# Optimization experiments

Hardware: AMD Instinct MI355X
Metric: run time of the kernel (lower is better)

The kernel has to match this reference:

```python
import jax, jax.numpy as jnp
import numpy as np

EMBED_DIM = 384
NUM_HEADS = 8
HEAD_DIM = EMBED_DIM // NUM_HEADS
GRN_EPS = 1e-6
LN_EPS = 1e-5


def grn(x, gamma, beta):
    # x: [B,C,H,W]; L2 norm over spatial dims per channel
    gx = jnp.sqrt(jnp.sum(x * x, axis=(-2, -1), keepdims=True))  # [B,C,1,1]
    nx = gx / (jnp.mean(gx, axis=-3, keepdims=True) + GRN_EPS)
    g = gamma[:, None, None]
    b = beta[:, None, None]
    return (1.0 + g) * (x * nx) + b + x


def layernorm(x, w, b):
    mu = jnp.mean(x, axis=-1, keepdims=True)
    var = jnp.mean(jnp.square(x - mu), axis=-1, keepdims=True)
    return (x - mu) * jax.lax.rsqrt(var + LN_EPS) * w + b


def setup_inputs() -> dict:
    key = jax.random.key(0)
    ks = jax.random.split(key, 16)
    C = EMBED_DIM
    B, Hq, Wq, Hk, Wk = 8, 64, 64, 32, 32
    s = 0.02
    inp = {
        "query_img": jax.random.normal(ks[0], (B, C, Hq, Wq), jnp.float32),
        "key_img": jax.random.normal(ks[1], (B, C, Hk, Wk), jnp.float32),
        "value_img": jax.random.normal(ks[2], (B, C, Hk, Wk), jnp.float32),
        "ada_gamma": jnp.zeros((C,), jnp.float32),
        "ada_beta": jnp.zeros((C,), jnp.float32),
        "Wq": jax.random.normal(ks[3], (C, C), jnp.float32) * s,
        "bq": jnp.zeros((C,), jnp.float32),
        "Wk": jax.random.normal(ks[4], (C, C), jnp.float32) * s,
        "bk": jnp.zeros((C,), jnp.float32),
        "Wv": jax.random.normal(ks[5], (C, C), jnp.float32) * s,
        "bv": jnp.zeros((C,), jnp.float32),
        "Wo": jax.random.normal(ks[6], (C, C), jnp.float32) * s,
        "bo": jnp.zeros((C,), jnp.float32),
        "lnq_w": jnp.ones((C,), jnp.float32),
        "lnq_b": jnp.zeros((C,), jnp.float32),
        "lnk_w": jnp.ones((C,), jnp.float32),
        "lnk_b": jnp.zeros((C,), jnp.float32),
        "attn_scalar": jnp.ones((C,), jnp.float32),
        "ffn_gamma": jnp.zeros((C,), jnp.float32),
        "ffn_beta": jnp.zeros((C,), jnp.float32),
        "W1": jax.random.normal(ks[7], (4 * C, C), jnp.float32) * s,
        "b1": jnp.zeros((4 * C,), jnp.float32),
        "W2": jax.random.normal(ks[8], (C, 4 * C), jnp.float32) * s,
        "b2": jnp.zeros((C,), jnp.float32),
        "ffn_scalar": jnp.ones((C,), jnp.float32),
        "final_scalar": jnp.ones((C,), jnp.float32) * 0.1,
    }
    return inp


def reference(query_img, key_img, value_img, ada_gamma, ada_beta, Wq, bq, Wk, bk,
              Wv, bv, Wo, bo, lnq_w, lnq_b, lnk_w, lnk_b, attn_scalar,
              ffn_gamma, ffn_beta, W1, b1, W2, b2, ffn_scalar, final_scalar):
    B, C, Hq, Wq_ = query_img.shape
    Nq = Hq * Wq_
    Nk = key_img.shape[2] * key_img.shape[3]
    H, D = NUM_HEADS, HEAD_DIM

    working = query_img
    ada = grn(working, ada_gamma, ada_beta)

    q_flat = ada.reshape(B, C, Nq).transpose(0, 2, 1)        # [B,Nq,C]
    k_flat = key_img.reshape(B, C, Nk).transpose(0, 2, 1)    # [B,Nk,C]
    v_flat = value_img.reshape(B, C, Nk).transpose(0, 2, 1)  # [B,Nk,C]

    q = layernorm(q_flat @ Wq.T + bq, lnq_w, lnq_b)
    k = layernorm(k_flat @ Wk.T + bk, lnk_w, lnk_b)
    v = v_flat @ Wv.T + bv

    q = (jax.nn.elu(q) + 1.0).reshape(B, Nq, H, D)
    k = (jax.nn.elu(k) + 1.0).reshape(B, Nk, H, D)
    v = v.reshape(B, Nk, H, D)

    kv_sum = jnp.einsum('bnhd,bnhe->bhde', k, v)   # [B,H,D,D]
    k_sum = jnp.sum(k, axis=1)                      # [B,H,D]
    num = jnp.einsum('bqhd,bhde->bqhe', q, kv_sum)  # [B,Nq,H,D]
    den = jnp.einsum('bqhd,bhd->bqh', q, k_sum)[..., None] + 1e-8
    attn = (num / den).reshape(B, Nq, C)
    attn = attn @ Wo.T + bo
    attn_out = attn.transpose(0, 2, 1).reshape(B, C, Hq, Wq_)

    working = working + attn_out * attn_scalar[None, :, None, None]

    normed = grn(working, ffn_gamma, ffn_beta)
    h = jnp.einsum('bchw,fc->bfhw', normed, W1) + b1[None, :, None, None]
    h = jax.nn.silu(h)
    ffn_out = jnp.einsum('bfhw,cf->bchw', h, W2) + b2[None, :, None, None]

    working = working + ffn_out * ffn_scalar[None, :, None, None]
    return query_img + working * final_scalar[None, :, None, None]
```

## Files before the change

### kernel.cpp

```cpp
#include <hip/hip_runtime.h>
#include <hip/hip_bf16.h>
#include <cmath>

typedef __hip_bfloat16 bf16;
typedef __attribute__((ext_vector_type(8))) short s16x8;
typedef __attribute__((ext_vector_type(4))) float f32x4;

#define B_  8
#define C_  384
#define NQ  4096
#define NK  1024
#define NH  8
#define HD  48
#define F_  1536

__device__ __forceinline__ float bits2f(short s) {
    unsigned int u = ((unsigned int)(unsigned short)s) << 16;
    float f; __builtin_memcpy(&f, &u, 4); return f;
}
__device__ __forceinline__ short f2bits(float f) {
    bf16 h = __float2bfloat16(f);
    short s; __builtin_memcpy(&s, &h, 2); return s;
}

__device__ __forceinline__ void gload16(const bf16* g, bf16* l) {
    __builtin_amdgcn_global_load_lds(
        (const __attribute__((address_space(1))) void*)g,
        (__attribute__((address_space(3))) void*)l, 16, 0, 0);
}

__global__ __launch_bounds__(256)
void grn_gx(const float* __restrict__ x, float* __restrict__ gx, int nsp)
{
    size_t base = (size_t)blockIdx.x * nsp;
    float s = 0.0f;
    for (int i = threadIdx.x * 4; i < nsp; i += 256 * 4) {
        float4 v = *reinterpret_cast<const float4*>(&x[base + i]);
        s += v.x * v.x + v.y * v.y + v.z * v.z + v.w * v.w;
    }
    for (int m = 32; m; m >>= 1) s += __shfl_xor(s, m);
    __shared__ float sh[4];
    if ((threadIdx.x & 63) == 0) sh[threadIdx.x >> 6] = s;
    __syncthreads();
    if (threadIdx.x == 0) gx[blockIdx.x] = sqrtf(sh[0] + sh[1] + sh[2] + sh[3]);
}

__global__ __launch_bounds__(384)
void grn_scale(const float* __restrict__ gx, const float* __restrict__ gamma,
               float* __restrict__ scale)
{
    int b = blockIdx.x;
    int c = threadIdx.x;
    float g = gx[b * C_ + c];
    float s = g;
    for (int m = 32; m; m >>= 1) s += __shfl_xor(s, m);
    __shared__ float sh[6];
    if ((c & 63) == 0) sh[c >> 6] = s;
    __syncthreads();
    if (c == 0) {
        float t = 0.0f;
        for (int i = 0; i < 6; ++i) t += sh[i];
        sh[0] = t / (float)C_;
    }
    __syncthreads();
    float nx = g / (sh[0] + 1e-6f);
    scale[b * C_ + c] = (1.0f + gamma[c]) * nx + 1.0f;
}

__global__ __launch_bounds__(256)
void cvt_bf16(const float* __restrict__ src, bf16* __restrict__ dst, int n)
{
    int i = (blockIdx.x * 256 + threadIdx.x) * 8;
    if (i >= n) return;
    float4 a = *reinterpret_cast<const float4*>(src + i);
    float4 b = *reinterpret_cast<const float4*>(src + i + 4);
    s16x8 o;
    o[0] = f2bits(a.x); o[1] = f2bits(a.y); o[2] = f2bits(a.z); o[3] = f2bits(a.w);
    o[4] = f2bits(b.x); o[5] = f2bits(b.y); o[6] = f2bits(b.z); o[7] = f2bits(b.w);
    *reinterpret_cast<s16x8*>(dst + i) = o;
}

template<bool SCALED>
__global__ __launch_bounds__(256)
void t2b(const float* __restrict__ src, bf16* __restrict__ dst,
         const float* __restrict__ scale, const float* __restrict__ shift, int Msp)
{
    const int b = blockIdx.z, c0 = blockIdx.y * 64, m0 = blockIdx.x * 64;
    __shared__ float T[64][65];
    const int tr = threadIdx.x >> 6, tc = threadIdx.x & 63;
    const float* sp = src + ((size_t)b * C_ + c0) * Msp + m0;
#pragma unroll
    for (int i = 0; i < 16; ++i)
        T[i * 4 + tr][tc] = sp[(size_t)(i * 4 + tr) * Msp + tc];
    __syncthreads();
    const int c = c0 + tc;
    float scl = 1.0f, sh = 0.0f;
    if constexpr (SCALED) { scl = scale[b * C_ + c]; sh = shift[c]; }
    bf16* dp = dst + ((size_t)b * Msp + m0) * C_ + c;
#pragma unroll
    for (int i = 0; i < 16; ++i) {
        int m = i * 4 + tr;
        dp[(size_t)m * C_] = __float2bfloat16(T[tc][m] * scl + sh);
    }
}

template<int EPI>
__global__ __launch_bounds__(256)
void gemm_mfma(const bf16* __restrict__ A, const bf16* __restrict__ W,
               const float* __restrict__ bias, int N, int K, int Mspat,
               bf16* __restrict__ outB, float* __restrict__ outF,
               const float* __restrict__ query,
               const float* __restrict__ sc1, const float* __restrict__ sc2)
{
    __shared__ __align__(16) char smem_raw[33792];
    const int tid  = threadIdx.x;
    const int lane = tid & 63, wave = tid >> 6;
    const int wm = wave >> 1, wn = wave & 1;
    const int lrow = lane & 15, lk8 = lane >> 4;
    const int mrow0 = blockIdx.x * 128;
    const int nt    = blockIdx.y * 128;

    const int r0   = wave * 32;
    const int srow = r0 + (lane >> 2);
    const int sk   = (lane & 3) * 8;
    const bf16* Ag = A + (size_t)(mrow0 + srow) * K + sk;
    const bf16* Wg = W + (size_t)(nt    + srow) * K + sk;
    f32x4 acc[4][4] = {};

    auto stage = [&](int p, int kt) {
        bf16* AsD = (bf16*)(smem_raw + p * 16384) + r0 * 32;
        bf16* BsD = (bf16*)(smem_raw + p * 16384 + 8192) + r0 * 32;
        gload16(Ag + kt,                  AsD);
        gload16(Ag + kt + (size_t)16 * K, AsD + 16 * 32);
        gload16(Wg + kt,                  BsD);
        gload16(Wg + kt + (size_t)16 * K, BsD + 16 * 32);
    };
    auto compute = [&](int p) {
        const bf16* As = (const bf16*)(smem_raw + p * 16384);
        const bf16* Bs = (const bf16*)(smem_raw + p * 16384 + 8192);
        s16x8 af[4], bfr[4];
#pragma unroll
        for (int m = 0; m < 4; ++m)
            af[m] = *reinterpret_cast<const s16x8*>(As + (wm * 64 + m * 16 + lrow) * 32 + lk8 * 8);
#pragma unroll
        for (int n = 0; n < 4; ++n)
            bfr[n] = *reinterpret_cast<const s16x8*>(Bs + (wn * 64 + n * 16 + lrow) * 32 + lk8 * 8);
#pragma unroll
        for (int m = 0; m < 4; ++m)
#pragma unroll
            for (int n = 0; n < 4; ++n)
                acc[m][n] = __builtin_amdgcn_mfma_f32_16x16x32_bf16(af[m], bfr[n], acc[m][n], 0, 0, 0);
    };

    stage(0, 0);
    stage(1, 32);
    int cur = 0;
    for (int kt = 0; kt < K - 32; kt += 32) {
        asm volatile("s_waitcnt vmcnt(4)" ::: "memory");
        __builtin_amdgcn_sched_barrier(0);
        __builtin_amdgcn_s_barrier();
        compute(cur);
        __builtin_amdgcn_s_barrier();
        if (kt + 64 < K) stage(cur, kt + 64);
        cur ^= 1;
    }
    asm volatile("s_waitcnt vmcnt(0)" ::: "memory");
    __builtin_amdgcn_sched_barrier(0);
    __builtin_amdgcn_s_barrier();
    compute(cur);
    __syncthreads();

    if constexpr (EPI <= 1) {
        bf16* Cs = (bf16*)smem_raw;
#pragma unroll
        for (int m = 0; m < 4; ++m)
#pragma unroll
            for (int n = 0; n < 4; ++n) {
                int col = wn * 64 + n * 16 + lrow;
                float bv = bias[nt + col];
#pragma unroll
                for (int j = 0; j < 4; ++j) {
                    int row = wm * 64 + m * 16 + lk8 * 4 + j;
                    float v = acc[m][n][j] + bv;
                    if constexpr (EPI == 1) v = v / (1.0f + __expf(-v));
                    Cs[row * 128 + col] = __float2bfloat16(v);
                }
            }
        __syncthreads();
#pragma unroll
        for (int p = 0; p < 8; ++p) {
            int e = p * 256 + tid;
            int row = e >> 4, ch = (e & 15) * 8;
            *reinterpret_cast<s16x8*>(outB + (size_t)(mrow0 + row) * N + nt + ch) =
                *reinterpret_cast<const s16x8*>(Cs + row * 128 + ch);
        }
    } else {
        float* Cs2 = (float*)smem_raw;
        const int b = mrow0 / Mspat;
        const int mloc0 = mrow0 - b * Mspat;
        for (int half = 0; half < 2; ++half) {
            if (half) __syncthreads();
            if (wn == half) {
#pragma unroll
                for (int m = 0; m < 4; ++m)
#pragma unroll
                    for (int n = 0; n < 4; ++n) {
                        int crow = n * 16 + lrow;
                        float bv = bias[nt + half * 64 + crow];
#pragma unroll
                        for (int j = 0; j < 4; ++j) {
                            int mcol = wm * 64 + m * 16 + lk8 * 4 + j;
                            Cs2[crow * 132 + mcol] = acc[m][n][j] + bv;
                        }
                    }
            }
            __syncthreads();
#pragma unroll
            for (int p = 0; p < 8; ++p) {
                int e = p * 256 + tid;
                int crow = e >> 5, m4 = (e & 31) * 4;
                int c = nt + half * 64 + crow;
                size_t off = ((size_t)b * C_ + c) * Mspat + mloc0 + m4;
                float4 v  = *reinterpret_cast<const float4*>(Cs2 + crow * 132 + m4);
                float4 q4 = *reinterpret_cast<const float4*>(query + off);
                float s1 = sc1[c];
                float4 o;
                if constexpr (EPI == 2) {
                    o.x = q4.x + v.x * s1;
                    o.y = q4.y + v.y * s1;
                    o.z = q4.z + v.z * s1;
                    o.w = q4.w + v.w * s1;
                } else {
                    float4 w4 = *reinterpret_cast<const float4*>(outF + off);
                    float s2 = sc2[c];
                    o.x = q4.x + (w4.x + v.x * s1) * s2;
                    o.y = q4.y + (w4.y + v.y * s1) * s2;
                    o.z = q4.z + (w4.z + v.z * s1) * s2;
                    o.w = q4.w + (w4.w + v.w * s1) * s2;
                }
                *reinterpret_cast<float4*>(outF + off) = o;
            }
        }
    }
}

__global__ __launch_bounds__(256)
void ln_elu_b(bf16* __restrict__ x, const float* __restrict__ w,
              const float* __restrict__ bb)
{
    int lane = threadIdx.x & 63, wid = threadIdx.x >> 6;
    int row = blockIdx.x * 4 + wid;
    bf16* p = x + (size_t)row * C_;
    float v[6];
#pragma unroll
    for (int i = 0; i < 6; ++i) v[i] = __bfloat162float(p[lane + i * 64]);
    float s = 0.0f;
#pragma unroll
    for (int i = 0; i < 6; ++i) s += v[i];
    for (int m = 32; m; m >>= 1) s += __shfl_xor(s, m);
    float mu = s / (float)C_;
    float vs = 0.0f;
#pragma unroll
    for (int i = 0; i < 6; ++i) { float d = v[i] - mu; vs += d * d; }
    for (int m = 32; m; m >>= 1) vs += __shfl_xor(vs, m);
    float inv = rsqrtf(vs / (float)C_ + 1e-5f);
#pragma unroll
    for (int i = 0; i < 6; ++i) {
        int c = lane + i * 64;
        float y = (v[i] - mu) * inv * w[c] + bb[c];
        p[c] = __float2bfloat16((y > 0.0f) ? (y + 1.0f) : __expf(y));
    }
}

__global__ __launch_bounds__(256)
void kv_reduce(const bf16* __restrict__ kn, const bf16* __restrict__ vn,
               float* __restrict__ kv, float* __restrict__ ksum)
{
    const int h = blockIdx.x, b = blockIdx.y;
    __shared__ float Ks[128][48];
    __shared__ float Vs[128][48];
    const int t = threadIdx.x;
    const int d0 = (t >> 4) * 3, e0 = (t & 15) * 3;
    float acc[3][3] = {};
    float ks[3] = {};
    for (int n0 = 0; n0 < NK; n0 += 128) {
        for (int ch = t; ch < 768; ch += 256) {
            int r = ch / 6, cc = (ch % 6) * 8;
            size_t base = ((size_t)(b * NK + n0 + r)) * C_ + h * HD + cc;
            s16x8 k8 = *reinterpret_cast<const s16x8*>(kn + base);
            s16x8 v8 = *reinterpret_cast<const s16x8*>(vn + base);
#pragma unroll
            for (int j = 0; j < 8; ++j) {
                Ks[r][cc + j] = bits2f(k8[j]);
                Vs[r][cc + j] = bits2f(v8[j]);
            }
        }
        __syncthreads();
#pragma unroll 4
        for (int r = 0; r < 128; ++r) {
            float k0 = Ks[r][d0], k1 = Ks[r][d0 + 1], k2 = Ks[r][d0 + 2];
            float v0 = Vs[r][e0], v1 = Vs[r][e0 + 1], v2 = Vs[r][e0 + 2];
            acc[0][0] = fmaf(k0, v0, acc[0][0]);
            acc[0][1] = fmaf(k0, v1, acc[0][1]);
            acc[0][2] = fmaf(k0, v2, acc[0][2]);
            acc[1][0] = fmaf(k1, v0, acc[1][0]);
            acc[1][1] = fmaf(k1, v1, acc[1][1]);
            acc[1][2] = fmaf(k1, v2, acc[1][2]);
            acc[2][0] = fmaf(k2, v0, acc[2][0]);
            acc[2][1] = fmaf(k2, v1, acc[2][1]);
            acc[2][2] = fmaf(k2, v2, acc[2][2]);
            if (e0 == 0) { ks[0] += k0; ks[1] += k1; ks[2] += k2; }
        }
        __syncthreads();
    }
    size_t base = (size_t)(b * NH + h) * HD;
#pragma unroll
    for (int i = 0; i < 3; ++i)
#pragma unroll
        for (int j = 0; j < 3; ++j)
            kv[(base + d0 + i) * HD + e0 + j] = acc[i][j];
    if (e0 == 0) {
#pragma unroll
        for (int i = 0; i < 3; ++i) ksum[base + d0 + i] = ks[i];
    }
}

__global__ __launch_bounds__(64)
void attn_numden(const bf16* __restrict__ q, const float* __restrict__ kv,
                 const float* __restrict__ ksum, bf16* __restrict__ attn)
{
    const int nc = blockIdx.x, h = blockIdx.y, b = blockIdx.z;
    __shared__ float skv[48 * 48];
    __shared__ float kss[48];
    const int t = threadIdx.x;
    const float* kvp = kv + (size_t)(b * NH + h) * HD * HD;
    for (int i = t; i < HD * HD; i += 64) skv[i] = kvp[i];
    if (t < HD) kss[t] = ksum[(size_t)(b * NH + h) * HD + t];
    __syncthreads();

    const int n = nc * 64 + t;
    const bf16* qp = q + ((size_t)b * NQ + n) * C_ + h * HD;
    float qv[48];
#pragma unroll
    for (int i = 0; i < 6; ++i) {
        s16x8 v = *reinterpret_cast<const s16x8*>(qp + i * 8);
#pragma unroll
        for (int j = 0; j < 8; ++j) qv[i * 8 + j] = bits2f(v[j]);
    }
    float num[48] = {};
    float den = 0.0f;
#pragma unroll 4
    for (int d = 0; d < 48; ++d) {
        float qd = qv[d];
        den = fmaf(qd, kss[d], den);
#pragma unroll
        for (int e = 0; e < 48; ++e) num[e] = fmaf(qd, skv[d * 48 + e], num[e]);
    }
    float inv = 1.0f / (den + 1e-8f);
    bf16* ap = attn + ((size_t)b * NQ + n) * C_ + h * HD;
#pragma unroll
    for (int i = 0; i < 6; ++i) {
        s16x8 o;
#pragma unroll
        for (int j = 0; j < 8; ++j) o[j] = f2bits(num[i * 8 + j] * inv);
        *reinterpret_cast<s16x8*>(ap + i * 8) = o;
    }
}

extern "C" void kernel_launch(void* const* d_in, const int* in_sizes, int n_in,
                              void* d_out, int out_size, void* d_ws, size_t ws_size,
                              hipStream_t stream)
{
    const float* query       = (const float*)d_in[0];
    const float* key         = (const float*)d_in[1];
    const float* value       = (const float*)d_in[2];
    const float* ada_gamma   = (const float*)d_in[3];
    const float* ada_beta    = (const float*)d_in[4];
    const float* Wq          = (const float*)d_in[5];
    const float* bq          = (const float*)d_in[6];
    const float* Wk          = (const float*)d_in[7];
    const float* bk          = (const float*)d_in[8];
    const float* Wv          = (const float*)d_in[9];
    const float* bv          = (const float*)d_in[10];
    const float* Wo          = (const float*)d_in[11];
    const float* bo          = (const float*)d_in[12];
    const float* lnq_w       = (const float*)d_in[13];
    const float* lnq_b       = (const float*)d_in[14];
    const float* lnk_w       = (const float*)d_in[15];
    const float* lnk_b       = (const float*)d_in[16];
    const float* attn_scalar = (const float*)d_in[17];
    const float* ffn_gamma   = (const float*)d_in[18];
    const float* ffn_beta    = (const float*)d_in[19];
    const float* W1          = (const float*)d_in[20];
    const float* b1          = (const float*)d_in[21];
    const float* W2          = (const float*)d_in[22];
    const float* b2          = (const float*)d_in[23];
    const float* ffn_scalar  = (const float*)d_in[24];
    const float* final_scalar= (const float*)d_in[25];
    float* out = (float*)d_out;

    float* ws    = (float*)d_ws;
    bf16* qbuf   = (bf16*)(ws);
    bf16* attnb  = (bf16*)(ws + 6291456);
    bf16* kbuf   = (bf16*)(ws + 12582912);
    bf16* vbuf   = (bf16*)(ws + 14155776);
    bf16* Akb    = (bf16*)(ws + 15728640);
    bf16* Avb    = (bf16*)(ws + 17301504);
    bf16* Aqb    = (bf16*)(ws + 18874368);
    bf16* hbuf   = (bf16*)(ws);
    bf16* Awb    = (bf16*)(ws + 25165824);
    bf16* wqb    = (bf16*)(ws + 31457280);
    bf16* wkb    = wqb + 147456;
    bf16* wvb    = wkb + 147456;
    bf16* wob    = wvb + 147456;
    bf16* w1b    = wob + 147456;
    bf16* w2b    = w1b + 589824;
    float* kvbuf = ws + 32342016;
    float* ksbuf = kvbuf + 147456;
    float* gx1   = ksbuf + 3072;
    float* sc1b  = gx1 + 3072;
    float* gx2   = sc1b + 3072;
    float* sc2b  = gx2 + 3072;

    cvt_bf16<<<72, 256, 0, stream>>>(Wq, wqb, 147456);
    cvt_bf16<<<72, 256, 0, stream>>>(Wk, wkb, 147456);
    cvt_bf16<<<72, 256, 0, stream>>>(Wv, wvb, 147456);
    cvt_bf16<<<72, 256, 0, stream>>>(Wo, wob, 147456);
    cvt_bf16<<<288, 256, 0, stream>>>(W1, w1b, 589824);
    cvt_bf16<<<288, 256, 0, stream>>>(W2, w2b, 589824);

    grn_gx<<<B_ * C_, 256, 0, stream>>>(query, gx1, NQ);
    grn_scale<<<B_, 384, 0, stream>>>(gx1, ada_gamma, sc1b);

    t2b<true ><<<dim3(64, 6, B_), 256, 0, stream>>>(query, Aqb, sc1b, ada_beta, NQ);
    t2b<false><<<dim3(16, 6, B_), 256, 0, stream>>>(key,   Akb, nullptr, nullptr, NK);
    t2b<false><<<dim3(16, 6, B_), 256, 0, stream>>>(value, Avb, nullptr, nullptr, NK);

    gemm_mfma<0><<<dim3(256, 3), 256, 0, stream>>>(Aqb, wqb, bq, 384, 384, NQ,
        qbuf, nullptr, nullptr, nullptr, nullptr);
    gemm_mfma<0><<<dim3(64, 3), 256, 0, stream>>>(Akb, wkb, bk, 384, 384, NK,
        kbuf, nullptr, nullptr, nullptr, nullptr);
    gemm_mfma<0><<<dim3(64, 3), 256, 0, stream>>>(Avb, wvb, bv, 384, 384, NK,
        vbuf, nullptr, nullptr, nullptr, nullptr);

    ln_elu_b<<<8192, 256, 0, stream>>>(qbuf, lnq_w, lnq_b);
    ln_elu_b<<<2048, 256, 0, stream>>>(kbuf, lnk_w, lnk_b);

    kv_reduce<<<dim3(NH, B_), 256, 0, stream>>>(kbuf, vbuf, kvbuf, ksbuf);
    attn_numden<<<dim3(NQ / 64, NH, B_), 64, 0, stream>>>(qbuf, kvbuf, ksbuf, attnb);

    gemm_mfma<2><<<dim3(256, 3), 256, 0, stream>>>(attnb, wob, bo, 384, 384, NQ,
        nullptr, out, query, attn_scalar, nullptr);

    grn_gx<<<B_ * C_, 256, 0, stream>>>(out, gx2, NQ);
    grn_scale<<<B_, 384, 0, stream>>>(gx2, ffn_gamma, sc2b);
    t2b<true><<<dim3(64, 6, B_), 256, 0, stream>>>(out, Awb, sc2b, ffn_beta, NQ);

    gemm_mfma<1><<<dim3(256, 12), 256, 0, stream>>>(Awb, w1b, b1, 1536, 384, NQ,
        hbuf, nullptr, nullptr, nullptr, nullptr);

    gemm_mfma<3><<<dim3(256, 3), 256, 0, stream>>>(hbuf, w2b, b2, 384, 1536, NQ,
        nullptr, out, query, ffn_scalar, final_scalar);
}
```

Baseline: 554.0 us.

## Enlarge GEMM tile to 256x128 with 8x4 MFMA accumulators per wave

The MFMA GEMM tile grows from 128x128 to 256x128 rows per block. Each wave now holds 8x4 accumulators and reuses each B fragment across 8 A fragments, which halves B-tile reloads per output. Shared memory and the epilogues are restructured into staged halves and quarters, and all GEMM grids are halved in x. The cost is higher register pressure and fewer blocks, which hurts occupancy and load balance on the smaller K and V GEMMs (96 blocks).

```diff
diff --git a/kernel.cpp b/kernel.cpp
--- a/kernel.cpp
+++ b/kernel.cpp
@@ -105,112 +105,83 @@
 }
 
 template<int EPI>
-__global__ __launch_bounds__(256)
+__global__ __launch_bounds__(256, 2)
 void gemm_mfma(const bf16* __restrict__ A, const bf16* __restrict__ W,
                const float* __restrict__ bias, int N, int K, int Mspat,
                bf16* __restrict__ outB, float* __restrict__ outF,
                const float* __restrict__ query,
                const float* __restrict__ sc1, const float* __restrict__ sc2)
 {
-    __shared__ __align__(16) char smem_raw[33792];
+    __shared__ __align__(16) char smem[49152];
     const int tid  = threadIdx.x;
     const int lane = tid & 63, wave = tid >> 6;
     const int wm = wave >> 1, wn = wave & 1;
     const int lrow = lane & 15, lk8 = lane >> 4;
-    const int mrow0 = blockIdx.x * 128;
+    const int mrow0 = blockIdx.x * 256;
     const int nt    = blockIdx.y * 128;
 
-    const int r0   = wave * 32;
-    const int srow = r0 + (lane >> 2);
-    const int sk   = (lane & 3) * 8;
-    const bf16* Ag = A + (size_t)(mrow0 + srow) * K + sk;
-    const bf16* Wg = W + (size_t)(nt    + srow) * K + sk;
-    f32x4 acc[4][4] = {};
+    const int sk = (lane & 3) * 8;
+    const bf16* Ag = A + (size_t)(mrow0 + wave * 64 + (lane >> 2)) * K + sk;
+    const bf16* Wg = W + (size_t)(nt    + wave * 32 + (lane >> 2)) * K + sk;
+    f32x4 acc[8][4] = {};
 
     auto stage = [&](int p, int kt) {
-        bf16* AsD = (bf16*)(smem_raw + p * 16384) + r0 * 32;
-        bf16* BsD = (bf16*)(smem_raw + p * 16384 + 8192) + r0 * 32;
-        gload16(Ag + kt,                  AsD);
-        gload16(Ag + kt + (size_t)16 * K, AsD + 16 * 32);
-        gload16(Wg + kt,                  BsD);
-        gload16(Wg + kt + (size_t)16 * K, BsD + 16 * 32);
+        bf16* Ad = (bf16*)(smem + p * 24576) + wave * 64 * 32;
+        bf16* Bd = (bf16*)(smem + p * 24576) + 8192 + wave * 32 * 32;
+#pragma unroll
+        for (int h = 0; h < 4; ++h)
+            gload16(Ag + kt + (size_t)(h * 16) * K, Ad + h * 512);
+#pragma unroll
+        for (int h = 0; h < 2; ++h)
+            gload16(Wg + kt + (size_t)(h * 16) * K, Bd + h * 512);
     };
     auto compute = [&](int p) {
-        const bf16* As = (const bf16*)(smem_raw + p * 16384);
-        const bf16* Bs = (const bf16*)(smem_raw + p * 16384 + 8192);
-        s16x8 af[4], bfr[4];
-#pragma unroll
-        for (int m = 0; m < 4; ++m)
-            af[m] = *reinterpret_cast<const s16x8*>(As + (wm * 64 + m * 16 + lrow) * 32 + lk8 * 8);
-#pragma unroll
-        for (int n = 0; n < 4; ++n)
-            bfr[n] = *reinterpret_cast<const s16x8*>(Bs + (wn * 64 + n * 16 + lrow) * 32 + lk8 * 8);
-#pragma unroll
-        for (int m = 0; m < 4; ++m)
-#pragma unroll
-            for (int n = 0; n < 4; ++n)
-                acc[m][n] = __builtin_amdgcn_mfma_f32_16x16x32_bf16(af[m], bfr[n], acc[m][n], 0, 0, 0);
+        const bf16* As = (const bf16*)(smem + p * 24576);
+        const bf16* Bs = As + 8192;
+        s16x8 af[8];
+#pragma unroll
+        for (int m = 0; m < 8; ++m)
+            af[m] = *reinterpret_cast<const s16x8*>(As + (wm * 128 + m * 16 + lrow) * 32 + lk8 * 8);
+#pragma unroll
+        for (int n = 0; n < 4; ++n) {
+            s16x8 bfr = *reinterpret_cast<const s16x8*>(Bs + (wn * 64 + n * 16 + lrow) * 32 + lk8 * 8);
+#pragma unroll
+            for (int m = 0; m < 8; ++m)
+                acc[m][n] = __builtin_amdgcn_mfma_f32_16x16x32_bf16(af[m], bfr, acc[m][n], 0, 0, 0);
+        }
     };
 
+    const int NT = K >> 5;
     stage(0, 0);
     stage(1, 32);
-    int cur = 0;
-    for (int kt = 0; kt < K - 32; kt += 32) {
-        asm volatile("s_waitcnt vmcnt(4)" ::: "memory");
+    for (int t = 0; t < NT; ++t) {
+        if (t < NT - 1) asm volatile("s_waitcnt vmcnt(6)" ::: "memory");
+        else            asm volatile("s_waitcnt vmcnt(0)" ::: "memory");
         __builtin_amdgcn_sched_barrier(0);
         __builtin_amdgcn_s_barrier();
-        compute(cur);
+        compute(t & 1);
         __builtin_amdgcn_s_barrier();
-        if (kt + 64 < K) stage(cur, kt + 64);
-        cur ^= 1;
-    }
-    asm volatile("s_waitcnt vmcnt(0)" ::: "memory");
-    __builtin_amdgcn_sched_barrier(0);
-    __builtin_amdgcn_s_barrier();
-    compute(cur);
+        if (t + 2 < NT) stage(t & 1, (t + 2) * 32);
+    }
     __syncthreads();
 
     if constexpr (EPI <= 1) {
-        bf16* Cs = (bf16*)smem_raw;
-#pragma unroll
-        for (int m = 0; m < 4; ++m)
-#pragma unroll
-            for (int n = 0; n < 4; ++n) {
-                int col = wn * 64 + n * 16 + lrow;
-                float bv = bias[nt + col];
-#pragma unroll
-                for (int j = 0; j < 4; ++j) {
-                    int row = wm * 64 + m * 16 + lk8 * 4 + j;
-                    float v = acc[m][n][j] + bv;
-                    if constexpr (EPI == 1) v = v / (1.0f + __expf(-v));
-                    Cs[row * 128 + col] = __float2bfloat16(v);
-                }
-            }
-        __syncthreads();
-#pragma unroll
-        for (int p = 0; p < 8; ++p) {
-            int e = p * 256 + tid;
-            int row = e >> 4, ch = (e & 15) * 8;
-            *reinterpret_cast<s16x8*>(outB + (size_t)(mrow0 + row) * N + nt + ch) =
-                *reinterpret_cast<const s16x8*>(Cs + row * 128 + ch);
-        }
-    } else {
-        float* Cs2 = (float*)smem_raw;
-        const int b = mrow0 / Mspat;
-        const int mloc0 = mrow0 - b * Mspat;
+        bf16* Cs = (bf16*)smem;
         for (int half = 0; half < 2; ++half) {
             if (half) __syncthreads();
-            if (wn == half) {
-#pragma unroll
-                for (int m = 0; m < 4; ++m)
+            if (wm == half) {
+#pragma unroll
+                for (int m = 0; m < 8; ++m)
 #pragma unroll
                     for (int n = 0; n < 4; ++n) {
-                        int crow = n * 16 + lrow;
-                        float bv = bias[nt + half * 64 + crow];
+                        int col = wn * 64 + n * 16 + lrow;
+                        float bv = bias[nt + col];
 #pragma unroll
                         for (int j = 0; j < 4; ++j) {
-                            int mcol = wm * 64 + m * 16 + lk8 * 4 + j;
-                            Cs2[crow * 132 + mcol] = acc[m][n][j] + bv;
+                            int row = m * 16 + lk8 * 4 + j;
+                            float v = acc[m][n][j] + bv;
+                            if constexpr (EPI == 1) v = v / (1.0f + __expf(-v));
+                            Cs[row * 128 + col] = __float2bfloat16(v);
                         }
                     }
             }
@@ -218,10 +189,40 @@
 #pragma unroll
             for (int p = 0; p < 8; ++p) {
                 int e = p * 256 + tid;
-                int crow = e >> 5, m4 = (e & 31) * 4;
-                int c = nt + half * 64 + crow;
+                int row = e >> 4, ch = (e & 15) * 8;
+                *reinterpret_cast<s16x8*>(
+                    outB + (size_t)(mrow0 + half * 128 + row) * N + nt + ch) =
+                    *reinterpret_cast<const s16x8*>(Cs + row * 128 + ch);
+            }
+        }
+    } else {
+        float* Ls = (float*)smem;
+        const int b = mrow0 / Mspat;
+        const int mloc0 = mrow0 - b * Mspat;
+        for (int s = 0; s < 4; ++s) {
+            if (s) __syncthreads();
+            if (wn == (s >> 1)) {
+#pragma unroll
+                for (int np = 0; np < 2; ++np) {
+                    int n = (s & 1) * 2 + np;
+                    int chl = np * 16 + lrow;
+                    float bv = bias[nt + s * 32 + chl];
+#pragma unroll
+                    for (int m = 0; m < 8; ++m)
+#pragma unroll
+                        for (int j = 0; j < 4; ++j)
+                            Ls[chl * 264 + wm * 128 + m * 16 + lk8 * 4 + j] =
+                                acc[m][n][j] + bv;
+                }
+            }
+            __syncthreads();
+#pragma unroll
+            for (int p = 0; p < 8; ++p) {
+                int e = p * 256 + tid;
+                int chl = e >> 6, m4 = (e & 63) * 4;
+                int c = nt + s * 32 + chl;
                 size_t off = ((size_t)b * C_ + c) * Mspat + mloc0 + m4;
-                float4 v  = *reinterpret_cast<const float4*>(Cs2 + crow * 132 + m4);
+                float4 v  = *reinterpret_cast<const float4*>(Ls + chl * 264 + m4);
                 float4 q4 = *reinterpret_cast<const float4*>(query + off);
                 float s1 = sc1[c];
                 float4 o;
@@ -436,11 +437,11 @@
     t2b<false><<<dim3(16, 6, B_), 256, 0, stream>>>(key,   Akb, nullptr, nullptr, NK);
     t2b<false><<<dim3(16, 6, B_), 256, 0, stream>>>(value, Avb, nullptr, nullptr, NK);
 
-    gemm_mfma<0><<<dim3(256, 3), 256, 0, stream>>>(Aqb, wqb, bq, 384, 384, NQ,
+    gemm_mfma<0><<<dim3(128, 3), 256, 0, stream>>>(Aqb, wqb, bq, 384, 384, NQ,
         qbuf, nullptr, nullptr, nullptr, nullptr);
-    gemm_mfma<0><<<dim3(64, 3), 256, 0, stream>>>(Akb, wkb, bk, 384, 384, NK,
+    gemm_mfma<0><<<dim3(32, 3), 256, 0, stream>>>(Akb, wkb, bk, 384, 384, NK,
         kbuf, nullptr, nullptr, nullptr, nullptr);
-    gemm_mfma<0><<<dim3(64, 3), 256, 0, stream>>>(Avb, wvb, bv, 384, 384, NK,
+    gemm_mfma<0><<<dim3(32, 3), 256, 0, stream>>>(Avb, wvb, bv, 384, 384, NK,
         vbuf, nullptr, nullptr, nullptr, nullptr);
 
     ln_elu_b<<<8192, 256, 0, stream>>>(qbuf, lnq_w, lnq_b);
@@ -449,16 +450,16 @@
     kv_reduce<<<dim3(NH, B_), 256, 0, stream>>>(kbuf, vbuf, kvbuf, ksbuf);
     attn_numden<<<dim3(NQ / 64, NH, B_), 64, 0, stream>>>(qbuf, kvbuf, ksbuf, attnb);
 
-    gemm_mfma<2><<<dim3(256, 3), 256, 0, stream>>>(attnb, wob, bo, 384, 384, NQ,
+    gemm_mfma<2><<<dim3(128, 3), 256, 0, stream>>>(attnb, wob, bo, 384, 384, NQ,
         nullptr, out, query, attn_scalar, nullptr);
 
     grn_gx<<<B_ * C_, 256, 0, stream>>>(out, gx2, NQ);
     grn_scale<<<B_, 384, 0, stream>>>(gx2, ffn_gamma, sc2b);
     t2b<true><<<dim3(64, 6, B_), 256, 0, stream>>>(out, Awb, sc2b, ffn_beta, NQ);
 
-    gemm_mfma<1><<<dim3(256, 12), 256, 0, stream>>>(Awb, w1b, b1, 1536, 384, NQ,
+    gemm_mfma<1><<<dim3(128, 12), 256, 0, stream>>>(Awb, w1b, b1, 1536, 384, NQ,
         hbuf, nullptr, nullptr, nullptr, nullptr);
 
-    gemm_mfma<3><<<dim3(256, 3), 256, 0, stream>>>(hbuf, w2b, b2, 384, 1536, NQ,
+    gemm_mfma<3><<<dim3(128, 3), 256, 0, stream>>>(hbuf, w2b, b2, 384, 1536, NQ,
         nullptr, out, query, ffn_scalar, final_scalar);
 }
```

Measured after the change: 585.7 us. 1.06x slower.
